# Kernel tuning notes

Hardware: AMD Instinct MI355X
Metric: run time of the kernel (lower is better)

Reference implementation:

```python
import jax, jax.numpy as jnp
import numpy as np

N = 50000   # nodes
E = 800000  # edges
D = 512     # channels (hidden_dim*2 == input_dim)
B = 64      # graphs in batch
L = 4       # GCN layers
OUT = 2
EPS = 1e-5


def setup_inputs() -> dict:
    key = jax.random.key(0)
    ks = jax.random.split(key, 12)
    x = jax.random.normal(ks[0], (N, D), jnp.float32)
    edge_index = jax.random.randint(ks[1], (2, E), 0, N, dtype=jnp.int64)
    batch = jnp.sort(jax.random.randint(ks[2], (N,), 0, B, dtype=jnp.int64))
    same_date = jax.random.randint(ks[3], (E,), 0, 2, dtype=jnp.int64)
    # parameters: 4 stacked GCNConv layers (same shape), BN stats, final linear
    Wc = jax.random.normal(ks[4], (L, D, D), jnp.float32) / np.float32(np.sqrt(D))
    bc = jax.random.normal(ks[5], (L, D), jnp.float32) * 0.01
    gamma = 1.0 + 0.1 * jax.random.normal(ks[6], (L, D), jnp.float32)
    beta = 0.1 * jax.random.normal(ks[7], (L, D), jnp.float32)
    rmean = 0.1 * jax.random.normal(ks[8], (L, D), jnp.float32)
    rvar = 0.5 + jax.random.uniform(ks[9], (L, D), jnp.float32)
    Wlin = jax.random.normal(ks[10], (2 * D, OUT), jnp.float32) / np.float32(np.sqrt(2 * D))
    blin = jnp.zeros((OUT,), jnp.float32)
    return {"x": x, "edge_index": edge_index, "batch": batch, "same_date": same_date,
            "Wc": Wc, "bc": bc, "gamma": gamma, "beta": beta, "rmean": rmean,
            "rvar": rvar, "Wlin": Wlin, "blin": blin}


def reference(x, edge_index, batch, same_date, Wc, bc, gamma, beta, rmean, rvar, Wlin, blin):
    # edge weights: 1.0 if same_date else 0.7
    w = jnp.where(same_date == 1, jnp.float32(1.0), jnp.float32(0.7))
    # GCN normalization with added self-loops (fill value 1.0)
    loops = jnp.arange(N, dtype=edge_index.dtype)
    row = jnp.concatenate([edge_index[0], loops])  # sources
    col = jnp.concatenate([edge_index[1], loops])  # targets
    ew = jnp.concatenate([w, jnp.ones((N,), jnp.float32)])
    deg = jax.ops.segment_sum(ew, col, num_segments=N)          # in-degree (weighted)
    dis = jax.lax.rsqrt(jnp.maximum(deg, EPS))                   # deg >= 1 from self-loops
    norm = dis[row] * ew * dis[col]                              # [E+N]

    h = x
    for i in range(L):
        hw = h @ Wc[i]                                           # [N, D]
        msg = hw[row] * norm[:, None]                            # gather + scale
        agg = jax.ops.segment_sum(msg, col, num_segments=N) + bc[i]
        # BatchNorm (inference: running stats) + ReLU; dropout is identity in eval
        h = gamma[i] * (agg - rmean[i]) * jax.lax.rsqrt(rvar[i] + EPS) + beta[i]
        h = jax.nn.relu(h)

    counts = jax.ops.segment_sum(jnp.ones((N,), jnp.float32), batch, num_segments=B)
    x_mean = jax.ops.segment_sum(h, batch, num_segments=B) / jnp.maximum(counts, 1.0)[:, None]
    x_max = jax.ops.segment_max(h, batch, num_segments=B)
    x_max = jnp.where(jnp.isfinite(x_max), x_max, 0.0)           # guard empty graphs
    z = jnp.concatenate([x_mean, x_max], axis=1) @ Wlin + blin   # [B, OUT]
    return jax.nn.log_softmax(z, axis=1)
```

## Files before the change

### kernel.cpp

```cpp
#include <hip/hip_runtime.h>
#include <hip/hip_bf16.h>

#define NN 50000
#define EE 800000
#define DD 512
#define BB 64
#define LL 4
#define OUTC 2
#define EPSV 1e-5f

#define MTG 64
#define BKG 64
#define HV8 (NN * DD / 8)

typedef _Float16 halfx8 __attribute__((ext_vector_type(8)));
typedef float floatx4 __attribute__((ext_vector_type(4)));
typedef float floatx2 __attribute__((ext_vector_type(2)));

#if defined(__has_builtin)
#if __has_builtin(__builtin_amdgcn_cvt_pk_f32_fp8) && __has_builtin(__builtin_amdgcn_cvt_pk_fp8_f32)
#define HW_FP8 1
#endif
#endif

#ifdef HW_FP8
__device__ __forceinline__ floatx2 f8x2_lo(unsigned int u) {
    return __builtin_amdgcn_cvt_pk_f32_fp8(u, 0);
}
__device__ __forceinline__ floatx2 f8x2_hi(unsigned int u) {
    return __builtin_amdgcn_cvt_pk_f32_fp8(u, 1);
}
__device__ __forceinline__ unsigned int f8_pack_lo(float a, float b, unsigned int old) {
    return (unsigned int)__builtin_amdgcn_cvt_pk_fp8_f32(a, b, (int)old, 0);
}
__device__ __forceinline__ unsigned int f8_pack_hi(float a, float b, unsigned int old) {
    return (unsigned int)__builtin_amdgcn_cvt_pk_fp8_f32(a, b, (int)old, 1);
}
__device__ __forceinline__ unsigned char f8_enc1(float v) {
    return (unsigned char)(__builtin_amdgcn_cvt_pk_fp8_f32(v, v, 0, 0) & 0xff);
}
#else
__device__ __forceinline__ float f8_dec1(unsigned int b) {
    unsigned int s = b & 0x80u, e = (b >> 3) & 15u, m = b & 7u;
    float v = e ? __uint_as_float(((e + 120u) << 23) | (m << 20))
                : (float)m * 0.001953125f;
    return s ? -v : v;
}
__device__ __forceinline__ floatx2 f8x2_lo(unsigned int u) {
    floatx2 r; r[0] = f8_dec1(u & 0xffu); r[1] = f8_dec1((u >> 8) & 0xffu); return r;
}
__device__ __forceinline__ floatx2 f8x2_hi(unsigned int u) {
    floatx2 r; r[0] = f8_dec1((u >> 16) & 0xffu); r[1] = f8_dec1((u >> 24) & 0xffu); return r;
}
__device__ __forceinline__ unsigned char f8_enc1(float x) {
    unsigned int s = (__float_as_uint(x) >> 24) & 0x80u;
    float a = fabsf(x);
    if (a < 0.015625f) {
        int m = (int)(a * 512.0f + 0.5f);
        return (unsigned char)(s | (unsigned int)m);
    }
    unsigned int ab = __float_as_uint(a);
    int e = (int)(ab >> 23) - 127;
    unsigned int m23 = ab & 0x7fffffu;
    unsigned int r = m23 + 0x7ffffu + ((m23 >> 20) & 1u);
    if (r >= 0x800000u) { e++; r -= 0x800000u; }
    unsigned int m = r >> 20;
    if (e > 8 || (e == 8 && m >= 7u)) return (unsigned char)(s | 0x7eu);
    return (unsigned char)(s | ((unsigned int)(e + 7) << 3) | m);
}
__device__ __forceinline__ unsigned int f8_pack_lo(float a, float b, unsigned int old) {
    return (old & 0xffff0000u) | (unsigned int)f8_enc1(a) | ((unsigned int)f8_enc1(b) << 8);
}
__device__ __forceinline__ unsigned int f8_pack_hi(float a, float b, unsigned int old) {
    return (old & 0x0000ffffu) | ((unsigned int)f8_enc1(a) << 16) | ((unsigned int)f8_enc1(b) << 24);
}
#endif

__device__ __forceinline__ floatx4 mfma16h(halfx8 a, halfx8 b, floatx4 c) {
    return __builtin_amdgcn_mfma_f32_16x16x32_f16(a, b, c, 0, 0, 0);
}

__device__ __forceinline__ void ldg2lds16(const _Float16* g, _Float16* l) {
    __builtin_amdgcn_global_load_lds(
        (const __attribute__((address_space(1))) unsigned int*)g,
        (__attribute__((address_space(3))) unsigned int*)l, 16, 0, 0);
}


__global__ void k_prep(const float* __restrict__ x, const float* __restrict__ Wc,
                       const int* __restrict__ ei, const int* __restrict__ sd,
                       const float* __restrict__ bc, const float* __restrict__ gamma,
                       const float* __restrict__ beta, const float* __restrict__ rmean,
                       const float* __restrict__ rvar,
                       unsigned char* __restrict__ X8, _Float16* __restrict__ WT,
                       unsigned long long* __restrict__ degcnt,
                       float* __restrict__ scb, float* __restrict__ shb) {
    int i = blockIdx.x * blockDim.x + threadIdx.x;
    if (i < HV8) {
        const float4* xp = (const float4*)x + (size_t)i * 2;
        float4 v0 = xp[0], v1 = xp[1];
        unsigned int u0 = 0, u1 = 0;
        u0 = f8_pack_lo(v0.x, v0.y, u0);
        u0 = f8_pack_hi(v0.z, v0.w, u0);
        u1 = f8_pack_lo(v1.x, v1.y, u1);
        u1 = f8_pack_hi(v1.z, v1.w, u1);
        uint2 q; q.x = u0; q.y = u1;
        ((uint2*)X8)[i] = q;
    }
    if (i < LL * DD * DD) {
        int l = i >> 18;
        int rem = i & ((DD * DD) - 1);
        int n = rem >> 9;
        int k = rem & (DD - 1);
        WT[(l << 18) + (n << 9) + (k ^ ((n & 7) << 3))] =
            (_Float16)Wc[(l << 18) + (k << 9) + n];
    }
    if (i < LL * DD) {
        float rs = rsqrtf(rvar[i] + EPSV);
        float scv = gamma[i] * rs;
        scb[i] = scv;
        shb[i] = scv * (bc[i] - rmean[i]) + beta[i];
    }
    if ((i & 3) == 0) {
        int e = i >> 2;
        if (e < EE) {
            int c = ei[EE + e];
            unsigned long long v =
                0x100000000ull + (unsigned long long)((sd[e] == 1) ? 10u : 7u);
            atomicAdd(&degcnt[c], v);
        }
    }
}

__global__ void k_scan1(const unsigned long long* __restrict__ degcnt,
                        int* __restrict__ rowptr, int* __restrict__ bsum,
                        float* __restrict__ dis, const int* __restrict__ batch,
                        int* __restrict__ gstart, int* __restrict__ gend) {
    __shared__ int sh[256];
    const int t = threadIdx.x;
    const int i = blockIdx.x * 256 + t;
    int cntv = 0;
    if (i < NN) {
        unsigned long long dc = degcnt[i];
        cntv = (int)(dc >> 32);
        float degv = 0.1f * (float)(unsigned int)(dc & 0xffffffffu);
        dis[i] = rsqrtf(fmaxf(degv + 1.0f, EPSV));
        int g = batch[i];
        int gp = (i == 0) ? -1 : batch[i - 1];
        if (g != gp) gstart[g] = i;
        int gn = (i == NN - 1) ? BB : batch[i + 1];
        if (g != gn) gend[g] = i + 1;
    }
    sh[t] = cntv;
    __syncthreads();
    for (int off = 1; off < 256; off <<= 1) {
        int y = (t >= off) ? sh[t - off] : 0;
        __syncthreads();
        if (t >= off) sh[t] += y;
        __syncthreads();
    }
    if (i < NN) rowptr[i] = sh[t] - cntv;
    if (t == 255) bsum[blockIdx.x] = sh[255];
}

__global__ void k_scan2(int* __restrict__ bsum, int* __restrict__ rowptr, int nb) {
    __shared__ int sh[256];
    const int t = threadIdx.x;
    int v = (t < nb) ? bsum[t] : 0;
    sh[t] = v;
    __syncthreads();
    for (int off = 1; off < 256; off <<= 1) {
        int y = (t >= off) ? sh[t - off] : 0;
        __syncthreads();
        if (t >= off) sh[t] += y;
        __syncthreads();
    }
    if (t < nb) bsum[t] = sh[t] - v;
    if (t == 255) rowptr[NN] = sh[255];
}

__global__ void k_scan3(int* __restrict__ rowptr, const int* __restrict__ bsum) {
    int i = blockIdx.x * blockDim.x + threadIdx.x;
    if (i < NN) rowptr[i] += bsum[i >> 8];
}

__global__ void k_fill(const int* __restrict__ ei, const int* __restrict__ sd,
                       const float* __restrict__ dis, const int* __restrict__ rowptr,
                       int* __restrict__ fill, uint2* __restrict__ edges) {
    int e = blockIdx.x * blockDim.x + threadIdx.x;
    if (e >= EE) return;
    int s = ei[e];
    int c = ei[EE + e];
    float w = (sd[e] == 1) ? 1.0f : 0.7f;
    int p = rowptr[c] + atomicAdd(&fill[c], 1);
    uint2 ev;
    ev.x = (unsigned int)s;
    ev.y = __float_as_uint(dis[s] * w * dis[c]);
    edges[p] = ev;
}

__launch_bounds__(256)
__global__ void k_agg(const unsigned char* __restrict__ h8, const int* __restrict__ rowptr,
                      const uint2* __restrict__ edges,
                      const float* __restrict__ dis, _Float16* __restrict__ S) {
    const int n = blockIdx.x * 4 + (threadIdx.x >> 6);
    const int lane = threadIdx.x & 63;
    if (n >= NN) return;
    const float dn = dis[n];
    const float sw = dn * dn;
    uint2 q = ((const uint2*)(h8 + (size_t)n * DD))[lane];
    floatx2 acc[4];
    acc[0] = f8x2_lo(q.x) * sw;
    acc[1] = f8x2_hi(q.x) * sw;
    acc[2] = f8x2_lo(q.y) * sw;
    acc[3] = f8x2_hi(q.y) * sw;
    const int s0 = rowptr[n], s1 = rowptr[n + 1];
    int i = s0;
    for (; i + 8 <= s1; i += 8) {
        uint2 ev[8];
        uint2 qv[8];
#pragma unroll
        for (int u = 0; u < 8; u++) ev[u] = edges[i + u];
#pragma unroll
        for (int u = 0; u < 8; u++)
            qv[u] = ((const uint2*)(h8 + (size_t)ev[u].x * DD))[lane];
#pragma unroll
        for (int u = 0; u < 8; u++) {
            const float wv = __uint_as_float(ev[u].y);
            acc[0] += f8x2_lo(qv[u].x) * wv;
            acc[1] += f8x2_hi(qv[u].x) * wv;
            acc[2] += f8x2_lo(qv[u].y) * wv;
            acc[3] += f8x2_hi(qv[u].y) * wv;
        }
    }
    for (; i + 4 <= s1; i += 4) {
        uint2 ev[4];
        uint2 qv[4];
#pragma unroll
        for (int u = 0; u < 4; u++) ev[u] = edges[i + u];
#pragma unroll
        for (int u = 0; u < 4; u++)
            qv[u] = ((const uint2*)(h8 + (size_t)ev[u].x * DD))[lane];
#pragma unroll
        for (int u = 0; u < 4; u++) {
            const float wv = __uint_as_float(ev[u].y);
            acc[0] += f8x2_lo(qv[u].x) * wv;
            acc[1] += f8x2_hi(qv[u].x) * wv;
            acc[2] += f8x2_lo(qv[u].y) * wv;
            acc[3] += f8x2_hi(qv[u].y) * wv;
        }
    }
    for (; i < s1; i++) {
        uint2 ev = edges[i];
        uint2 qb = ((const uint2*)(h8 + (size_t)ev.x * DD))[lane];
        const float wn = __uint_as_float(ev.y);
        acc[0] += f8x2_lo(qb.x) * wn;
        acc[1] += f8x2_hi(qb.x) * wn;
        acc[2] += f8x2_lo(qb.y) * wn;
        acc[3] += f8x2_hi(qb.y) * wn;
    }
    halfx8 hv;
#pragma unroll
    for (int k = 0; k < 4; k++) {
        hv[2 * k] = (_Float16)acc[k][0];
        hv[2 * k + 1] = (_Float16)acc[k][1];
    }
    ((halfx8*)(S + (size_t)n * DD))[lane ^ (n & 7)] = hv;
}

template <int OUT8>
__launch_bounds__(512)
__global__ void k_gemm(const _Float16* __restrict__ A,
                       const _Float16* __restrict__ B,
                       const float* __restrict__ sc, const float* __restrict__ sh,
                       _Float16* __restrict__ C16, unsigned char* __restrict__ C8,
                       const int* __restrict__ batch,
                       float* __restrict__ psum, unsigned int* __restrict__ pmax) {
    __shared__ _Float16 sA[MTG * BKG];
    __shared__ _Float16 sB[512 * BKG];

    const int t = threadIdx.x;
    const int wid = t >> 6;
    const int lane = t & 63;
    const int l15 = lane & 15;
    const int quad = lane >> 4;
    const int m0 = blockIdx.x * MTG;
    const int wc = wid * 64;
    const int key = l15 & 7;

    int arow = m0 + (t >> 3);
    if (arow > NN - 1) arow = NN - 1;
    const _Float16* gA = A + (size_t)arow * DD + (t & 7) * 8;
    _Float16* lA = sA + t * 8;
    const _Float16* gB = B + (size_t)(t >> 3) * DD + (t & 7) * 8;
    _Float16* lB = sB + t * 8;

    floatx4 acc[4][4];
#pragma unroll
    for (int i = 0; i < 4; i++)
#pragma unroll
        for (int j = 0; j < 4; j++) acc[i][j] = (floatx4){0.f, 0.f, 0.f, 0.f};

    for (int k0 = 0; k0 < DD; k0 += BKG) {
        __syncthreads();
        ldg2lds16(gA + k0, lA);
#pragma unroll
        for (int r = 0; r < 8; r++)
            ldg2lds16(gB + (size_t)r * 64 * DD + k0, lB + r * 4096);
        __syncthreads();

#pragma unroll
        for (int cc = 0; cc < 2; cc++) {
            halfx8 a[4], b[4];
            const int goff = ((cc * 4 + quad) ^ key) * 8;
#pragma unroll
            for (int i = 0; i < 4; i++)
                a[i] = *(const halfx8*)&sA[(i * 16 + l15) * BKG + goff];
#pragma unroll
            for (int j = 0; j < 4; j++)
                b[j] = *(const halfx8*)&sB[(wc + j * 16 + l15) * BKG + goff];
#pragma unroll
            for (int i = 0; i < 4; i++)
#pragma unroll
                for (int j = 0; j < 4; j++)
                    acc[i][j] = mfma16h(a[i], b[j], acc[i][j]);
        }
    }

    __syncthreads();
    _Float16* bounce = sB;
    int* sgid = (int*)sA;
    if (!OUT8 && t < 64) {
        const int grow = m0 + t;
        sgid[t] = (grow < NN) ? batch[grow] : -1;
    }
#pragma unroll
    for (int j = 0; j < 4; j++) {
        const int gcol = wc + j * 16 + l15;
        const float scv = sc[gcol];
        const float shv = sh[gcol];
#pragma unroll
        for (int i = 0; i < 4; i++) {
#pragma unroll
            for (int r = 0; r < 4; r++) {
                const int row = i * 16 + quad * 4 + r;
                float v = fmaxf(fmaf(scv, acc[i][j][r], shv), 0.f);
                bounce[row * DD + (gcol ^ ((row & 7) << 3))] = (_Float16)v;
            }
        }
    }
    __syncthreads();
    if (OUT8) {
#pragma unroll
        for (int p = 0; p < 4; p++) {
            const int G = p * 512 + t;
            const int row = G >> 5;
            const int c = G & 31;
            const int rk = row & 7;
            const int g0 = (2 * c) ^ rk;
            halfx8 ha = *(const halfx8*)&bounce[row * DD + g0 * 8];
            halfx8 hb = *(const halfx8*)&bounce[row * DD + (g0 ^ 1) * 8];
            unsigned int u0 = 0, u1 = 0, u2 = 0, u3 = 0;
            u0 = f8_pack_lo((float)ha[0], (float)ha[1], u0);
            u0 = f8_pack_hi((float)ha[2], (float)ha[3], u0);
            u1 = f8_pack_lo((float)ha[4], (float)ha[5], u1);
            u1 = f8_pack_hi((float)ha[6], (float)ha[7], u1);
            u2 = f8_pack_lo((float)hb[0], (float)hb[1], u2);
            u2 = f8_pack_hi((float)hb[2], (float)hb[3], u2);
            u3 = f8_pack_lo((float)hb[4], (float)hb[5], u3);
            u3 = f8_pack_hi((float)hb[6], (float)hb[7], u3);
            const int grow = m0 + row;
            if (grow < NN) {
                uint4 qo; qo.x = u0; qo.y = u1; qo.z = u2; qo.w = u3;
                *(uint4*)(C8 + (size_t)grow * DD + c * 16) = qo;
            }
        }
    } else {
#pragma unroll
        for (int p = 0; p < 8; p++) {
            const int g = p * 512 + t;
            const int row = g >> 6;
            const int c8 = g & 63;
            const int grow = m0 + row;
            if (grow < NN) {
                halfx8 hv = *(const halfx8*)
                    &bounce[row * DD + ((c8 ^ (row & 7)) << 3)];
                *(halfx8*)(C16 + (size_t)grow * DD + c8 * 8) = hv;
            }
        }
        const int c = t;
        float sum = 0.f, mx = 0.f;
        int curg = sgid[0];
        for (int r = 0; r < MTG; r++) {
            if (m0 + r >= NN) break;
            const int gid = sgid[r];
            if (gid != curg) {
                atomicAdd(&psum[curg * DD + c], sum);
                atomicMax(&pmax[curg * DD + c], __float_as_uint(fmaxf(mx, 0.f)));
                sum = 0.f; mx = 0.f; curg = gid;
            }
            float v = (float)bounce[r * DD + (c ^ ((r & 7) << 3))];
            sum += v;
            mx = fmaxf(mx, v);
        }
        atomicAdd(&psum[curg * DD + c], sum);
        atomicMax(&pmax[curg * DD + c], __float_as_uint(fmaxf(mx, 0.f)));
    }
}

__launch_bounds__(64)
__global__ void k_final(const float* __restrict__ psum, const unsigned int* __restrict__ pmax,
                        const int* __restrict__ gstart, const int* __restrict__ gend,
                        const float* __restrict__ Wlin, const float* __restrict__ blin,
                        float* __restrict__ out) {
    const int g = blockIdx.x;
    const int lane = threadIdx.x;
    int cntg = gend[g] - gstart[g];
    if (cntg < 1) cntg = 1;
    const float inv = 1.0f / (float)cntg;
    float z0 = 0.f, z1 = 0.f;
#pragma unroll
    for (int j = 0; j < 8; j++) {
        const int k = j * 64 + lane;
        float mean = psum[g * DD + k] * inv;
        float mx = __uint_as_float(pmax[g * DD + k]);
        z0 += mean * Wlin[k * OUTC + 0] + mx * Wlin[(DD + k) * OUTC + 0];
        z1 += mean * Wlin[k * OUTC + 1] + mx * Wlin[(DD + k) * OUTC + 1];
    }
#pragma unroll
    for (int off = 32; off > 0; off >>= 1) {
        z0 += __shfl_down(z0, off);
        z1 += __shfl_down(z1, off);
    }
    if (lane == 0) {
        z0 += blin[0];
        z1 += blin[1];
        float m = fmaxf(z0, z1);
        float ls = m + logf(expf(z0 - m) + expf(z1 - m));
        out[g * OUTC + 0] = z0 - ls;
        out[g * OUTC + 1] = z1 - ls;
    }
}

extern "C" void kernel_launch(void* const* d_in, const int* in_sizes, int n_in,
                              void* d_out, int out_size, void* d_ws, size_t ws_size,
                              hipStream_t stream) {
    const float* x = (const float*)d_in[0];
    const int* ei = (const int*)d_in[1];
    const int* batch = (const int*)d_in[2];
    const int* sd = (const int*)d_in[3];
    const float* Wc = (const float*)d_in[4];
    const float* bc = (const float*)d_in[5];
    const float* gamma = (const float*)d_in[6];
    const float* beta = (const float*)d_in[7];
    const float* rmean = (const float*)d_in[8];
    const float* rvar = (const float*)d_in[9];
    const float* Wlin = (const float*)d_in[10];
    const float* blin = (const float*)d_in[11];
    float* out = (float*)d_out;

    char* p = (char*)d_ws;
    auto alloc = [&](size_t bytes) {
        char* r = p;
        p += (bytes + 255) & ~(size_t)255;
        return r;
    };
    _Float16* S = (_Float16*)alloc((size_t)NN * DD * 2);
    unsigned char* X8a = (unsigned char*)alloc((size_t)NN * DD);
    unsigned char* X8b = (unsigned char*)alloc((size_t)NN * DD);
    _Float16* WT = (_Float16*)alloc((size_t)LL * DD * DD * 2);
    float* scb = (float*)alloc(LL * DD * 4);
    float* shb = (float*)alloc(LL * DD * 4);
    uint2* edges = (uint2*)alloc((size_t)EE * 8);
    char* zbase = p;
    unsigned long long* degcnt = (unsigned long long*)alloc(NN * 8);
    float* dis = (float*)alloc(NN * 4);
    int* fill = (int*)alloc(NN * 4);
    int* rowptr = (int*)alloc((NN + 1) * 4);
    int* bsum = (int*)alloc(256 * 4);
    int* gstart = (int*)alloc(BB * 4);
    int* gend = (int*)alloc(BB * 4);
    float* psum = (float*)alloc(BB * DD * 4);
    unsigned int* pmax = (unsigned int*)alloc(BB * DD * 4);
    size_t zbytes = (size_t)(p - zbase);
    (void)ws_size; (void)in_sizes; (void)n_in; (void)out_size;

    const int nb256 = (NN + 255) / 256;
    const int eb256 = (EE + 255) / 256;

    hipMemsetAsync(zbase, 0, zbytes, stream);
    k_prep<<<(HV8 + 255) / 256, 256, 0, stream>>>(x, Wc, ei, sd, bc, gamma, beta,
                                                  rmean, rvar, X8a, WT, degcnt, scb, shb);
    k_scan1<<<nb256, 256, 0, stream>>>(degcnt, rowptr, bsum, dis, batch, gstart, gend);
    k_scan2<<<1, 256, 0, stream>>>(bsum, rowptr, nb256);
    k_scan3<<<nb256, 256, 0, stream>>>(rowptr, bsum);
    k_fill<<<eb256, 256, 0, stream>>>(ei, sd, dis, rowptr, fill, edges);

    const int ggrid = (NN + MTG - 1) / MTG;
    unsigned char* bufs[2] = {X8a, X8b};
    int cur = 0;
    for (int l = 0; l < LL; l++) {
        k_agg<<<(NN + 3) / 4, 256, 0, stream>>>(bufs[cur], rowptr, edges, dis, S);
        if (l < LL - 1)
            k_gemm<1><<<ggrid, 512, 0, stream>>>(S, WT + (size_t)l * DD * DD,
                                                 scb + l * DD, shb + l * DD,
                                                 nullptr, bufs[cur ^ 1],
                                                 nullptr, nullptr, nullptr);
        else
            k_gemm<0><<<ggrid, 512, 0, stream>>>(S, WT + (size_t)l * DD * DD,
                                                 scb + l * DD, shb + l * DD,
                                                 S, nullptr,
                                                 batch, psum, pmax);
        cur ^= 1;
    }

    k_final<<<BB, 64, 0, stream>>>(psum, pmax, gstart, gend, Wlin, blin, out);
}
```

Measured before the change: 649.1 us.

## Retile GEMM to 128x256 blocks split over column halves, drop fp16 output store

```diff
diff --git a/kernel.cpp b/kernel.cpp
--- a/kernel.cpp
+++ b/kernel.cpp
@@ -9,7 +9,6 @@
 #define OUTC 2
 #define EPSV 1e-5f
 
-#define MTG 64
 #define BKG 64
 #define HV8 (NN * DD / 8)
 
@@ -35,9 +34,6 @@
 }
 __device__ __forceinline__ unsigned int f8_pack_hi(float a, float b, unsigned int old) {
     return (unsigned int)__builtin_amdgcn_cvt_pk_fp8_f32(a, b, (int)old, 1);
-}
-__device__ __forceinline__ unsigned char f8_enc1(float v) {
-    return (unsigned char)(__builtin_amdgcn_cvt_pk_fp8_f32(v, v, 0, 0) & 0xff);
 }
 #else
 __device__ __forceinline__ float f8_dec1(unsigned int b) {
@@ -273,26 +269,33 @@
 __global__ void k_gemm(const _Float16* __restrict__ A,
                        const _Float16* __restrict__ B,
                        const float* __restrict__ sc, const float* __restrict__ sh,
-                       _Float16* __restrict__ C16, unsigned char* __restrict__ C8,
+                       unsigned char* __restrict__ C8,
                        const int* __restrict__ batch,
                        float* __restrict__ psum, unsigned int* __restrict__ pmax) {
-    __shared__ _Float16 sA[MTG * BKG];
-    __shared__ _Float16 sB[512 * BKG];
+    __shared__ _Float16 sA[128 * 64];
+    __shared__ _Float16 sB[256 * 64];
 
     const int t = threadIdx.x;
     const int wid = t >> 6;
     const int lane = t & 63;
     const int l15 = lane & 15;
     const int quad = lane >> 4;
-    const int m0 = blockIdx.x * MTG;
-    const int wc = wid * 64;
+    const int rb = blockIdx.x >> 1;
+    const int ch = blockIdx.x & 1;
+    const int m0 = rb * 128;
+    const int n0 = ch * 256;
+    const int wr = wid >> 2;
+    const int wcg = wid & 3;
     const int key = l15 & 7;
 
-    int arow = m0 + (t >> 3);
-    if (arow > NN - 1) arow = NN - 1;
-    const _Float16* gA = A + (size_t)arow * DD + (t & 7) * 8;
+    int ar0 = m0 + (t >> 3);
+    int ar1 = m0 + 64 + (t >> 3);
+    if (ar0 > NN - 1) ar0 = NN - 1;
+    if (ar1 > NN - 1) ar1 = NN - 1;
+    const _Float16* gA0 = A + (size_t)ar0 * DD + (t & 7) * 8;
+    const _Float16* gA1 = A + (size_t)ar1 * DD + (t & 7) * 8;
+    const _Float16* gB = B + (size_t)(n0 + (t >> 3)) * DD + (t & 7) * 8;
     _Float16* lA = sA + t * 8;
-    const _Float16* gB = B + (size_t)(t >> 3) * DD + (t & 7) * 8;
     _Float16* lB = sB + t * 8;
 
     floatx4 acc[4][4];
@@ -303,9 +306,10 @@
 
     for (int k0 = 0; k0 < DD; k0 += BKG) {
         __syncthreads();
-        ldg2lds16(gA + k0, lA);
-#pragma unroll
-        for (int r = 0; r < 8; r++)
+        ldg2lds16(gA0 + k0, lA);
+        ldg2lds16(gA1 + k0, lA + 4096);
+#pragma unroll
+        for (int r = 0; r < 4; r++)
             ldg2lds16(gB + (size_t)r * 64 * DD + k0, lB + r * 4096);
         __syncthreads();
 
@@ -315,10 +319,10 @@
             const int goff = ((cc * 4 + quad) ^ key) * 8;
 #pragma unroll
             for (int i = 0; i < 4; i++)
-                a[i] = *(const halfx8*)&sA[(i * 16 + l15) * BKG + goff];
+                a[i] = *(const halfx8*)&sA[(wr * 64 + i * 16 + l15) * 64 + goff];
 #pragma unroll
             for (int j = 0; j < 4; j++)
-                b[j] = *(const halfx8*)&sB[(wc + j * 16 + l15) * BKG + goff];
+                b[j] = *(const halfx8*)&sB[(wcg * 64 + j * 16 + l15) * 64 + goff];
 #pragma unroll
             for (int i = 0; i < 4; i++)
 #pragma unroll
@@ -330,81 +334,81 @@
     __syncthreads();
     _Float16* bounce = sB;
     int* sgid = (int*)sA;
-    if (!OUT8 && t < 64) {
+    if (!OUT8 && t < 128) {
         const int grow = m0 + t;
         sgid[t] = (grow < NN) ? batch[grow] : -1;
     }
-#pragma unroll
-    for (int j = 0; j < 4; j++) {
-        const int gcol = wc + j * 16 + l15;
-        const float scv = sc[gcol];
-        const float shv = sh[gcol];
-#pragma unroll
-        for (int i = 0; i < 4; i++) {
-#pragma unroll
-            for (int r = 0; r < 4; r++) {
-                const int row = i * 16 + quad * 4 + r;
-                float v = fmaxf(fmaf(scv, acc[i][j][r], shv), 0.f);
-                bounce[row * DD + (gcol ^ ((row & 7) << 3))] = (_Float16)v;
+    float sum = 0.f, mx = 0.f;
+    int curg = 0;
+#pragma unroll
+    for (int p = 0; p < 2; p++) {
+        if (p) __syncthreads();
+        if (wr == p) {
+#pragma unroll
+            for (int j = 0; j < 4; j++) {
+                const int gcl = wcg * 64 + j * 16 + l15;
+                const float scv = sc[n0 + gcl];
+                const float shv = sh[n0 + gcl];
+#pragma unroll
+                for (int i = 0; i < 4; i++) {
+#pragma unroll
+                    for (int r = 0; r < 4; r++) {
+                        const int row = i * 16 + quad * 4 + r;
+                        float v = fmaxf(fmaf(scv, acc[i][j][r], shv), 0.f);
+                        bounce[row * 256 + (gcl ^ ((row & 7) << 3))] = (_Float16)v;
+                    }
+                }
             }
         }
-    }
-    __syncthreads();
-    if (OUT8) {
-#pragma unroll
-        for (int p = 0; p < 4; p++) {
-            const int G = p * 512 + t;
-            const int row = G >> 5;
-            const int c = G & 31;
-            const int rk = row & 7;
-            const int g0 = (2 * c) ^ rk;
-            halfx8 ha = *(const halfx8*)&bounce[row * DD + g0 * 8];
-            halfx8 hb = *(const halfx8*)&bounce[row * DD + (g0 ^ 1) * 8];
-            unsigned int u0 = 0, u1 = 0, u2 = 0, u3 = 0;
-            u0 = f8_pack_lo((float)ha[0], (float)ha[1], u0);
-            u0 = f8_pack_hi((float)ha[2], (float)ha[3], u0);
-            u1 = f8_pack_lo((float)ha[4], (float)ha[5], u1);
-            u1 = f8_pack_hi((float)ha[6], (float)ha[7], u1);
-            u2 = f8_pack_lo((float)hb[0], (float)hb[1], u2);
-            u2 = f8_pack_hi((float)hb[2], (float)hb[3], u2);
-            u3 = f8_pack_lo((float)hb[4], (float)hb[5], u3);
-            u3 = f8_pack_hi((float)hb[6], (float)hb[7], u3);
-            const int grow = m0 + row;
-            if (grow < NN) {
-                uint4 qo; qo.x = u0; qo.y = u1; qo.z = u2; qo.w = u3;
-                *(uint4*)(C8 + (size_t)grow * DD + c * 16) = qo;
+        __syncthreads();
+        if (OUT8) {
+#pragma unroll
+            for (int it = 0; it < 2; it++) {
+                const int idx = it * 512 + t;
+                const int row = idx >> 4;
+                const int c = idx & 15;
+                const int rk = row & 7;
+                const int g0 = (2 * c) ^ rk;
+                halfx8 ha = *(const halfx8*)&bounce[row * 256 + g0 * 8];
+                halfx8 hb = *(const halfx8*)&bounce[row * 256 + (g0 ^ 1) * 8];
+                unsigned int u0 = 0, u1 = 0, u2 = 0, u3 = 0;
+                u0 = f8_pack_lo((float)ha[0], (float)ha[1], u0);
+                u0 = f8_pack_hi((float)ha[2], (float)ha[3], u0);
+                u1 = f8_pack_lo((float)ha[4], (float)ha[5], u1);
+                u1 = f8_pack_hi((float)ha[6], (float)ha[7], u1);
+                u2 = f8_pack_lo((float)hb[0], (float)hb[1], u2);
+                u2 = f8_pack_hi((float)hb[2], (float)hb[3], u2);
+                u3 = f8_pack_lo((float)hb[4], (float)hb[5], u3);
+                u3 = f8_pack_hi((float)hb[6], (float)hb[7], u3);
+                const int grow = m0 + p * 64 + row;
+                if (grow < NN) {
+                    uint4 qo; qo.x = u0; qo.y = u1; qo.z = u2; qo.w = u3;
+                    *(uint4*)(C8 + (size_t)grow * DD + n0 + c * 16) = qo;
+                }
+            }
+        } else {
+            if (t < 256) {
+                if (p == 0) curg = sgid[0];
+                for (int r = 0; r < 64; r++) {
+                    const int grow = m0 + p * 64 + r;
+                    if (grow >= NN) break;
+                    const int gid = sgid[p * 64 + r];
+                    if (gid != curg) {
+                        atomicAdd(&psum[curg * DD + n0 + t], sum);
+                        atomicMax(&pmax[curg * DD + n0 + t],
+                                  __float_as_uint(fmaxf(mx, 0.f)));
+                        sum = 0.f; mx = 0.f; curg = gid;
+                    }
+                    float v = (float)bounce[r * 256 + (t ^ ((r & 7) << 3))];
+                    sum += v;
+                    mx = fmaxf(mx, v);
+                }
             }
         }
-    } else {
-#pragma unroll
-        for (int p = 0; p < 8; p++) {
-            const int g = p * 512 + t;
-            const int row = g >> 6;
-            const int c8 = g & 63;
-            const int grow = m0 + row;
-            if (grow < NN) {
-                halfx8 hv = *(const halfx8*)
-                    &bounce[row * DD + ((c8 ^ (row & 7)) << 3)];
-                *(halfx8*)(C16 + (size_t)grow * DD + c8 * 8) = hv;
-            }
-        }
-        const int c = t;
-        float sum = 0.f, mx = 0.f;
-        int curg = sgid[0];
-        for (int r = 0; r < MTG; r++) {
-            if (m0 + r >= NN) break;
-            const int gid = sgid[r];
-            if (gid != curg) {
-                atomicAdd(&psum[curg * DD + c], sum);
-                atomicMax(&pmax[curg * DD + c], __float_as_uint(fmaxf(mx, 0.f)));
-                sum = 0.f; mx = 0.f; curg = gid;
-            }
-            float v = (float)bounce[r * DD + (c ^ ((r & 7) << 3))];
-            sum += v;
-            mx = fmaxf(mx, v);
-        }
-        atomicAdd(&psum[curg * DD + c], sum);
-        atomicMax(&pmax[curg * DD + c], __float_as_uint(fmaxf(mx, 0.f)));
+    }
+    if (!OUT8 && t < 256) {
+        atomicAdd(&psum[curg * DD + n0 + t], sum);
+        atomicMax(&pmax[curg * DD + n0 + t], __float_as_uint(fmaxf(mx, 0.f)));
     }
 }
 
@@ -496,7 +500,7 @@
     k_scan3<<<nb256, 256, 0, stream>>>(rowptr, bsum);
     k_fill<<<eb256, 256, 0, stream>>>(ei, sd, dis, rowptr, fill, edges);
 
-    const int ggrid = (NN + MTG - 1) / MTG;
+    const int ggrid = 2 * ((NN + 127) / 128);
     unsigned char* bufs[2] = {X8a, X8b};
     int cur = 0;
     for (int l = 0; l < LL; l++) {
@@ -504,12 +508,12 @@
         if (l < LL - 1)
             k_gemm<1><<<ggrid, 512, 0, stream>>>(S, WT + (size_t)l * DD * DD,
                                                  scb + l * DD, shb + l * DD,
-                                                 nullptr, bufs[cur ^ 1],
+                                                 bufs[cur ^ 1],
                                                  nullptr, nullptr, nullptr);
         else
             k_gemm<0><<<ggrid, 512, 0, stream>>>(S, WT + (size_t)l * DD * DD,
                                                  scb + l * DD, shb + l * DD,
-                                                 S, nullptr,
+                                                 nullptr,
                                                  batch, psum, pmax);
         cur ^= 1;
     }
```

After: 672.3 us. 3.6% more time.
